# Kernel tuning notes

Hardware: AMD Instinct MI355X
Metric: run time of the kernel (lower is better)

The kernel has to match this reference:

```python
import jax, jax.numpy as jnp
import numpy as np

LN_EPS = 1e-5

def _conv2d(x, w, b, pad):
    # x: [B,C,H,W], w: [O,I,kh,kw] -> [B,O,H,W]
    y = jax.lax.conv_general_dilated(
        x, w, window_strides=(1, 1), padding=[(pad, pad), (pad, pad)],
        dimension_numbers=('NCHW', 'OIHW', 'NCHW'))
    return y + b[None, :, None, None]

def setup_inputs() -> dict:
    key = jax.random.key(0)
    ks = jax.random.split(key, 12)
    B, C, H, W = 4, 256, 64, 64
    D = 64  # inner_projection
    s_in = 1.0 / np.sqrt(C)
    s_d1 = 1.0 / np.sqrt(D)
    s_d3 = 1.0 / np.sqrt(D * 9)
    return {
        'x':     jax.random.normal(ks[0], (B, C, H, W), jnp.float32),
        'w_in':  jax.random.normal(ks[1], (D, C, 1, 1), jnp.float32) * s_in,
        'b_in':  jnp.zeros((D,), jnp.float32),
        'wq':    jax.random.normal(ks[2], (D, D, 3, 3), jnp.float32) * s_d3,
        'bq':    jnp.zeros((D,), jnp.float32),
        'wk':    jax.random.normal(ks[3], (D, D, 3, 3), jnp.float32) * s_d3,
        'bk':    jnp.zeros((D,), jnp.float32),
        'wv':    jax.random.normal(ks[4], (D, D, 3, 3), jnp.float32) * s_d3,
        'bv':    jnp.zeros((D,), jnp.float32),
        'w_out': jax.random.normal(ks[5], (C, D, 1, 1), jnp.float32) * s_d1,
        'b_out': jnp.zeros((C,), jnp.float32),
        'gamma': jax.random.normal(ks[6], (1,), jnp.float32) * 0.1,
        'ln_w':  jnp.ones((C,), jnp.float32),
        'ln_b':  jnp.zeros((C,), jnp.float32),
    }

def _attention(q, k, v):
    # full-pixel attention, NO 1/sqrt(d) scale (matches source)
    B, C, H, W = v.shape
    N = H * W
    qf = q.reshape(B, -1, N)   # [B,d,N]
    kf = k.reshape(B, -1, N)
    vf = v.reshape(B, -1, N)
    energy = jnp.einsum('bci,bcj->bij', qf, kf)      # [B,N,N] = Q^T K
    attn = jax.nn.softmax(energy, axis=-1)
    out = jnp.einsum('bcj,bij->bci', vf, attn)        # V @ attn^T
    return out.reshape(B, C, H, W)

def _layernorm2d(x, w, b):
    # normalize over channel dim per pixel (LayerNorm2d)
    mu = jnp.mean(x, axis=1, keepdims=True)
    var = jnp.var(x, axis=1, keepdims=True)
    xn = (x - mu) * jax.lax.rsqrt(var + LN_EPS)
    return xn * w[None, :, None, None] + b[None, :, None, None]

def reference(x, w_in, b_in, wq, bq, wk, bk, wv, bv, w_out, b_out, gamma, ln_w, ln_b):
    att = _conv2d(x, w_in, b_in, 0)          # inner projection [B,D,H,W]
    q = _conv2d(att, wq, bq, 1)
    k = _conv2d(att, wk, bk, 1)
    v = _conv2d(att, wv, bv, 1)
    att = _attention(q, k, v)
    att = _conv2d(att, w_out, b_out, 0)       # outer projection [B,C,H,W]
    return _layernorm2d(gamma * x + att, ln_w, ln_b)
```

## Files before the change

### kernel.cpp

```cpp
#include <hip/hip_runtime.h>
#include <hip/hip_bf16.h>

#define BB 4
#define CC 256
#define DD 64
#define HH 64
#define WW 64
#define NN 4096
#define NSPLIT 8
#define SM_SHIFT 64.0f

typedef __hip_bfloat16 bf16;
typedef __attribute__((ext_vector_type(8))) short bf16x8;
typedef __attribute__((ext_vector_type(4))) float f32x4;
typedef __attribute__((ext_vector_type(4))) short s16x4;

#define MFMA16(a, b, c) __builtin_amdgcn_mfma_f32_16x16x32_bf16(a, b, c, 0, 0, 0)

static __device__ __forceinline__ float ldin(const void* p, size_t i, bool isb) {
  return isb ? __bfloat162float(((const bf16*)p)[i]) : ((const float*)p)[i];
}
static __device__ __forceinline__ void stout(void* p, size_t i, float v, bool isb) {
  if (isb) ((bf16*)p)[i] = __float2bfloat16(v);
  else     ((float*)p)[i] = v;
}
static __device__ __forceinline__ unsigned pack2(bf16 a, bf16 b) {
  unsigned short ua = *reinterpret_cast<unsigned short*>(&a);
  unsigned short ub = *reinterpret_cast<unsigned short*>(&b);
  return (unsigned)ua | ((unsigned)ub << 16);
}
static __device__ __forceinline__ bool probe_bf16(const unsigned* lnw) {
  return lnw[0] == 0x3F803F80u;
}

__global__ __launch_bounds__(256) void k_wt(
    const void* __restrict__ wq, const void* __restrict__ wk,
    const void* __restrict__ wv, const void* __restrict__ w_in,
    const void* __restrict__ w_out,
    bf16* __restrict__ Wth, bf16* __restrict__ Wtl,
    bf16* __restrict__ Win_h, bf16* __restrict__ Win_l,
    bf16* __restrict__ Wo_h, bf16* __restrict__ Wo_l,
    const unsigned* __restrict__ lnw) {
  const bool isb = probe_bf16(lnw);
  int u = blockIdx.x * 256 + threadIdx.x;
  if (u < 110592) {
    int c3 = u / 36864, rem = u % 36864;
    int tap = rem / 4096, r2 = rem % 4096;
    int oc = r2 >> 6, ic = r2 & 63;
    const void* w = (c3 == 0) ? wq : ((c3 == 1) ? wk : wv);
    float v = ldin(w, (size_t)oc * 576 + ic * 9 + tap, isb);
    bf16 h = __float2bfloat16(v);
    Wth[u] = h;
    Wtl[u] = __float2bfloat16(v - __bfloat162float(h));
  } else if (u < 126976) {
    int v2 = u - 110592;
    float v = ldin(w_in, v2, isb);
    bf16 h = __float2bfloat16(v);
    Win_h[v2] = h;
    Win_l[v2] = __float2bfloat16(v - __bfloat162float(h));
  } else {
    int v2 = u - 126976;
    float v = ldin(w_out, v2, isb);
    bf16 h = __float2bfloat16(v);
    Wo_h[v2] = h;
    Wo_l[v2] = __float2bfloat16(v - __bfloat162float(h));
  }
}

__global__ __launch_bounds__(256) void k_conv_in(
    const void* __restrict__ x,
    const bf16* __restrict__ Win_h, const bf16* __restrict__ Win_l,
    const void* __restrict__ bias, bf16* __restrict__ att_h,
    bf16* __restrict__ att_l, const unsigned* __restrict__ lnw) {
  __shared__ __align__(16) short Xh[32 * 64];
  __shared__ __align__(16) short Xl[32 * 64];
  const bool isb = probe_bf16(lnw);
  const int b = blockIdx.y, n0 = blockIdx.x * 32;
  const int t = threadIdx.x;
  const int w = t >> 6, lane = t & 63, quad = lane >> 4, l16 = lane & 15;
  const int l7 = l16 & 7;
  const size_t xoff = (size_t)b * CC * NN;
  f32x4 acc[2];
  #pragma unroll
  for (int nt = 0; nt < 2; ++nt)
    #pragma unroll
    for (int r = 0; r < 4; ++r)
      acc[nt][r] = ldin(bias, w * 16 + quad * 4 + r, isb);
  for (int c0 = 0; c0 < CC; c0 += 64) {
    __syncthreads();
    #pragma unroll
    for (int i = 0; i < 4; ++i) {
      int u = t + i * 256;
      int dd = u >> 5, n = u & 31;
      float v0 = ldin(x, xoff + (size_t)(c0 + 2 * dd) * NN + n0 + n, isb);
      float v1 = ldin(x, xoff + (size_t)(c0 + 2 * dd + 1) * NN + n0 + n, isb);
      bf16 h0 = __float2bfloat16(v0), h1 = __float2bfloat16(v1);
      bf16 l0 = __float2bfloat16(v0 - __bfloat162float(h0));
      bf16 l1 = __float2bfloat16(v1 - __bfloat162float(h1));
      int cs = ((dd >> 2) ^ (n & 7)) * 8 + ((2 * dd) & 7);
      *(unsigned*)&Xh[n * 64 + cs] = pack2(h0, h1);
      *(unsigned*)&Xl[n * 64 + cs] = pack2(l0, l1);
    }
    __syncthreads();
    #pragma unroll
    for (int kc = 0; kc < 2; ++kc) {
      size_t woff = (size_t)(w * 16 + l16) * 256 + c0 + kc * 32 + quad * 8;
      bf16x8 wh = *(const bf16x8*)(Win_h + woff);
      bf16x8 wl = *(const bf16x8*)(Win_l + woff);
      const int xo = ((kc * 4 + quad) ^ l7) * 8;
      #pragma unroll
      for (int nt = 0; nt < 2; ++nt) {
        int rn = nt * 16 + l16;
        bf16x8 xh = *(const bf16x8*)&Xh[rn * 64 + xo];
        bf16x8 xl = *(const bf16x8*)&Xl[rn * 64 + xo];
        acc[nt] = MFMA16(wh, xh, acc[nt]);
        acc[nt] = MFMA16(wh, xl, acc[nt]);
        acc[nt] = MFMA16(wl, xh, acc[nt]);
      }
    }
  }
  #pragma unroll
  for (int nt = 0; nt < 2; ++nt) {
    size_t off = ((size_t)b * NN + n0 + nt * 16 + l16) * DD + w * 16 + quad * 4;
    bf16 h[4], l[4];
    #pragma unroll
    for (int r = 0; r < 4; ++r) {
      float v = acc[nt][r];
      h[r] = __float2bfloat16(v);
      l[r] = __float2bfloat16(v - __bfloat162float(h[r]));
    }
    *(uint2*)&att_h[off] = make_uint2(pack2(h[0], h[1]), pack2(h[2], h[3]));
    *(uint2*)&att_l[off] = make_uint2(pack2(l[0], l[1]), pack2(l[2], l[3]));
  }
}

__global__ __launch_bounds__(256) void k_conv3(
    const bf16* __restrict__ att_h, const bf16* __restrict__ att_l,
    const bf16* __restrict__ Wth, const bf16* __restrict__ Wtl,
    const void* __restrict__ bq, const void* __restrict__ bk,
    const void* __restrict__ bv,
    bf16* __restrict__ qth, bf16* __restrict__ qtl,
    bf16* __restrict__ kth, bf16* __restrict__ ktl,
    bf16* __restrict__ vt, const unsigned* __restrict__ lnw) {
  __shared__ __align__(16) short Ah[3 * 66 * 64];
  __shared__ __align__(16) short Al[3 * 66 * 64];
  float* o_s = reinterpret_cast<float*>(Ah);
  const bool isb = probe_bf16(lnw);
  const int y = blockIdx.x, b = blockIdx.y, c3 = blockIdx.z;
  const int t = threadIdx.x;
  const int w = t >> 6, lane = t & 63, quad = lane >> 4, l16 = lane & 15;
  const uint4 z4 = make_uint4(0, 0, 0, 0);
  #pragma unroll
  for (int r = 0; r < 3; ++r) {
    int yp = y + r - 1;
    bool ok = (unsigned)yp < 64u;
    const uint4* sh = (const uint4*)(att_h + ((size_t)b * NN + (size_t)yp * 64) * DD);
    const uint4* sl = (const uint4*)(att_l + ((size_t)b * NN + (size_t)yp * 64) * DD);
    #pragma unroll
    for (int ii = 0; ii < 2; ++ii) {
      int u = t + ii * 256;
      int xx = u >> 3, ch = u & 7;
      int rr = r * 66 + xx + 1;
      uint4 vh = ok ? sh[u] : z4;
      uint4 vl = ok ? sl[u] : z4;
      int cs = (ch ^ (rr & 7)) * 8;
      *(uint4*)&Ah[rr * 64 + cs] = vh;
      *(uint4*)&Al[rr * 64 + cs] = vl;
    }
    if (t < 16) {
      int rr = r * 66 + ((t & 1) ? 65 : 0);
      int cs = (t >> 1) * 8;
      *(uint4*)&Ah[rr * 64 + cs] = z4;
      *(uint4*)&Al[rr * 64 + cs] = z4;
    }
  }
  __syncthreads();
  const void* bp = (c3 == 0) ? bq : ((c3 == 1) ? bk : bv);
  const bf16* wth = Wth + (size_t)c3 * 9 * 4096;
  const bf16* wtl = Wtl + (size_t)c3 * 9 * 4096;
  f32x4 acc[4];
  #pragma unroll
  for (int nt = 0; nt < 4; ++nt)
    #pragma unroll
    for (int r = 0; r < 4; ++r)
      acc[nt][r] = ldin(bp, w * 16 + quad * 4 + r, isb);
  #pragma unroll
  for (int tap = 0; tap < 9; ++tap) {
    const int dy = tap / 3, dx = tap % 3;
    const int woff = tap * 4096 + (w * 16 + l16) * 64 + quad * 8;
    bf16x8 wh0 = *(const bf16x8*)(wth + woff);
    bf16x8 wh1 = *(const bf16x8*)(wth + woff + 32);
    bf16x8 wl0 = *(const bf16x8*)(wtl + woff);
    bf16x8 wl1 = *(const bf16x8*)(wtl + woff + 32);
    #pragma unroll
    for (int nt = 0; nt < 4; ++nt) {
      int rr = dy * 66 + nt * 16 + l16 + dx;
      int chA = (quad ^ (rr & 7)) * 8;
      int chB = ((quad + 4) ^ (rr & 7)) * 8;
      bf16x8 ah0 = *(const bf16x8*)&Ah[rr * 64 + chA];
      bf16x8 ah1 = *(const bf16x8*)&Ah[rr * 64 + chB];
      bf16x8 al0 = *(const bf16x8*)&Al[rr * 64 + chA];
      bf16x8 al1 = *(const bf16x8*)&Al[rr * 64 + chB];
      acc[nt] = MFMA16(wh0, ah0, acc[nt]);
      acc[nt] = MFMA16(wh1, ah1, acc[nt]);
      acc[nt] = MFMA16(wh0, al0, acc[nt]);
      acc[nt] = MFMA16(wh1, al1, acc[nt]);
      acc[nt] = MFMA16(wl0, ah0, acc[nt]);
      acc[nt] = MFMA16(wl1, ah1, acc[nt]);
    }
  }
  if (c3 < 2) {
    bf16* dh = (c3 == 0) ? qth : kth;
    bf16* dl = (c3 == 0) ? qtl : ktl;
    const size_t rowb = (size_t)b * NN + (size_t)y * 64;
    #pragma unroll
    for (int nt = 0; nt < 4; ++nt) {
      size_t off = (rowb + nt * 16 + l16) * DD + w * 16 + quad * 4;
      bf16 h[4], l[4];
      #pragma unroll
      for (int r = 0; r < 4; ++r) {
        float v = acc[nt][r];
        h[r] = __float2bfloat16(v);
        l[r] = __float2bfloat16(v - __bfloat162float(h[r]));
      }
      *(uint2*)&dh[off] = make_uint2(pack2(h[0], h[1]), pack2(h[2], h[3]));
      *(uint2*)&dl[off] = make_uint2(pack2(l[0], l[1]), pack2(l[2], l[3]));
    }
  } else {
    __syncthreads();
    #pragma unroll
    for (int nt = 0; nt < 4; ++nt)
      #pragma unroll
      for (int r = 0; r < 4; ++r)
        o_s[(nt * 16 + l16) * 65 + w * 16 + quad * 4 + r] = acc[nt][r];
    __syncthreads();
    #pragma unroll
    for (int i = 0; i < 8; ++i) {
      int u = t + i * 256;
      int c = u >> 5, np = (u & 31) * 2;
      float v0 = o_s[np * 65 + c], v1 = o_s[(np + 1) * 65 + c];
      *(unsigned*)&vt[((size_t)b * DD + c) * NN + (size_t)y * 64 + np] =
          pack2(__float2bfloat16(v0), __float2bfloat16(v1));
    }
  }
}

__global__ __launch_bounds__(256) void k_attn(
    const bf16* __restrict__ qth, const bf16* __restrict__ qtl,
    const bf16* __restrict__ kth, const bf16* __restrict__ ktl,
    const bf16* __restrict__ vt, float* __restrict__ po,
    float* __restrict__ pl) {
  __shared__ __align__(16) short Kh[64 * 64];
  __shared__ __align__(16) short Kl[64 * 64];
  __shared__ __align__(16) short Vs[64 * 64];
  __shared__ __align__(16) short Ps[64 * 64];
  const int b = blockIdx.y, i0 = blockIdx.x * 64, sp = blockIdx.z;
  const int jt0 = sp * (64 / NSPLIT), jt1 = jt0 + (64 / NSPLIT);
  const int t = threadIdx.x;
  const int w = t >> 6, lane = t & 63, quad = lane >> 4, l16 = lane & 15;
  const int l7 = l16 & 7;
  const int xA = (quad ^ l7) * 8;
  const int xB = ((quad + 4) ^ l7) * 8;
  const int sr = t >> 2, m4 = t & 3, sg = m4 * 16;
  const int sc0 = ((2 * m4) ^ (sr & 7)) * 8;
  const int sc1 = ((2 * m4 + 1) ^ (sr & 7)) * 8;
  {
    size_t off = ((size_t)b * NN + i0 + sr) * DD + sg;
    const uint4* qh = (const uint4*)(qth + off);
    const uint4* ql = (const uint4*)(qtl + off);
    *(uint4*)&Kh[sr * 64 + sc0] = qh[0];
    *(uint4*)&Kh[sr * 64 + sc1] = qh[1];
    *(uint4*)&Kl[sr * 64 + sc0] = ql[0];
    *(uint4*)&Kl[sr * 64 + sc1] = ql[1];
  }
  uint4 kh0, kh1, kl0, kl1, vx0, vx1;
  {
    size_t koff = ((size_t)b * NN + jt0 * 64 + sr) * DD + sg;
    kh0 = ((const uint4*)(kth + koff))[0]; kh1 = ((const uint4*)(kth + koff))[1];
    kl0 = ((const uint4*)(ktl + koff))[0]; kl1 = ((const uint4*)(ktl + koff))[1];
    size_t voff = ((size_t)b * DD + sr) * NN + jt0 * 64 + sg;
    vx0 = ((const uint4*)(vt + voff))[0];  vx1 = ((const uint4*)(vt + voff))[1];
  }
  __syncthreads();
  const int rq = w * 16 + l16;
  const bf16x8 qf_h0 = *(const bf16x8*)&Kh[rq * 64 + xA];
  const bf16x8 qf_h1 = *(const bf16x8*)&Kh[rq * 64 + xB];
  const bf16x8 qf_l0 = *(const bf16x8*)&Kl[rq * 64 + xA];
  const bf16x8 qf_l1 = *(const bf16x8*)&Kl[rq * 64 + xB];
  float l_run = 0.f;
  f32x4 oacc[4] = {};
  for (int jt = jt0; jt < jt1; ++jt) {
    __syncthreads();
    *(uint4*)&Kh[sr * 64 + sc0] = kh0;    *(uint4*)&Kh[sr * 64 + sc1] = kh1;
    *(uint4*)&Kl[sr * 64 + sc0] = kl0;    *(uint4*)&Kl[sr * 64 + sc1] = kl1;
    *(uint4*)&Vs[sr * 64 + sc0] = vx0;    *(uint4*)&Vs[sr * 64 + sc1] = vx1;
    __syncthreads();
    if (jt < jt1 - 1) {
      int j0n = (jt + 1) * 64;
      size_t koff = ((size_t)b * NN + j0n + sr) * DD + sg;
      kh0 = ((const uint4*)(kth + koff))[0]; kh1 = ((const uint4*)(kth + koff))[1];
      kl0 = ((const uint4*)(ktl + koff))[0]; kl1 = ((const uint4*)(ktl + koff))[1];
      size_t voff = ((size_t)b * DD + sr) * NN + j0n + sg;
      vx0 = ((const uint4*)(vt + voff))[0];  vx1 = ((const uint4*)(vt + voff))[1];
    }
    f32x4 s[4];
    #pragma unroll
    for (int mt = 0; mt < 4; ++mt) {
      int r0 = (mt * 16 + l16) * 64;
      bf16x8 kf_h0 = *(const bf16x8*)&Kh[r0 + xA];
      bf16x8 kf_h1 = *(const bf16x8*)&Kh[r0 + xB];
      bf16x8 kf_l0 = *(const bf16x8*)&Kl[r0 + xA];
      bf16x8 kf_l1 = *(const bf16x8*)&Kl[r0 + xB];
      f32x4 c = {0.f, 0.f, 0.f, 0.f};
      c = MFMA16(kf_h0, qf_h0, c);
      c = MFMA16(kf_h1, qf_h1, c);
      c = MFMA16(kf_h0, qf_l0, c);
      c = MFMA16(kf_h1, qf_l1, c);
      c = MFMA16(kf_l0, qf_h0, c);
      c = MFMA16(kf_l1, qf_h1, c);
      s[mt] = c;
    }
    float psum = 0.f;
    short pb[16];
    #pragma unroll
    for (int mt = 0; mt < 4; ++mt)
      #pragma unroll
      for (int r = 0; r < 4; ++r) {
        float p = __expf(s[mt][r] - SM_SHIFT);
        bf16 ph = __float2bfloat16(p);
        psum += __bfloat162float(ph);
        pb[mt * 4 + r] = *reinterpret_cast<short*>(&ph);
      }
    psum += __shfl_xor(psum, 16, 64);
    psum += __shfl_xor(psum, 32, 64);
    l_run += psum;
    #pragma unroll
    for (int mt = 0; mt < 4; ++mt) {
      s16x4 pk;
      pk.x = pb[mt * 4 + 0]; pk.y = pb[mt * 4 + 1];
      pk.z = pb[mt * 4 + 2]; pk.w = pb[mt * 4 + 3];
      int chP = ((2 * mt + (quad >> 1)) ^ l7) * 8 + (quad & 1) * 4;
      *(s16x4*)&Ps[rq * 64 + chP] = pk;
    }
    bf16x8 pf0 = *(const bf16x8*)&Ps[rq * 64 + xA];
    bf16x8 pf1 = *(const bf16x8*)&Ps[rq * 64 + xB];
    #pragma unroll
    for (int mt = 0; mt < 4; ++mt) {
      int r0 = (mt * 16 + l16) * 64;
      bf16x8 vf0 = *(const bf16x8*)&Vs[r0 + xA];
      bf16x8 vf1 = *(const bf16x8*)&Vs[r0 + xB];
      oacc[mt] = MFMA16(vf0, pf0, oacc[mt]);
      oacc[mt] = MFMA16(vf1, pf1, oacc[mt]);
    }
  }
  const int ig = i0 + w * 16 + l16;
  const size_t SEGC = (size_t)BB * DD * NN;
  #pragma unroll
  for (int mt = 0; mt < 4; ++mt)
    #pragma unroll
    for (int r = 0; r < 4; ++r) {
      int c = mt * 16 + quad * 4 + r;
      po[(size_t)sp * SEGC + ((size_t)b * DD + c) * NN + ig] = oacc[mt][r];
    }
  if (quad == 0) pl[((size_t)sp * BB + b) * NN + ig] = l_run;
}

__global__ __launch_bounds__(256) void k_out_ln(
    const float* __restrict__ po, const float* __restrict__ pl,
    const void* __restrict__ x,
    const bf16* __restrict__ Wo_h, const bf16* __restrict__ Wo_l,
    const void* __restrict__ bias, const void* __restrict__ gamma,
    const void* __restrict__ lw, const void* __restrict__ lb,
    void* __restrict__ out, const unsigned* __restrict__ lnw) {
  __shared__ __align__(16) short Ahs[32 * 64];
  __shared__ __align__(16) short Als[32 * 64];
  __shared__ float inv_s[32];
  __shared__ float red1[32 * 4], red2[32 * 4];
  __shared__ float mu_s[32], rs_s[32];
  __shared__ float lw_s[256], lb_s[256];
  const bool isb = probe_bf16(lnw);
  const int b = blockIdx.y, n0 = blockIdx.x * 32;
  const int t = threadIdx.x;
  const int w = t >> 6, lane = t & 63, quad = lane >> 4, l16 = lane & 15;
  const int l7 = l16 & 7;
  const size_t SEGC = (size_t)BB * DD * NN;
  if (t < 32) {
    int i = n0 + t;
    float lsum = 0.f;
    #pragma unroll
    for (int s = 0; s < NSPLIT; ++s) lsum += pl[((size_t)s * BB + b) * NN + i];
    inv_s[t] = 1.f / lsum;
  }
  lw_s[t] = ldin(lw, t, isb);
  lb_s[t] = ldin(lb, t, isb);
  const float g = ldin(gamma, 0, isb);
  __syncthreads();
  #pragma unroll
  for (int i = 0; i < 4; ++i) {
    int u = t + i * 256;
    int dd = u >> 5, n = u & 31;
    size_t base = ((size_t)b * DD + 2 * dd) * NN + n0 + n;
    float v0 = 0.f, v1 = 0.f;
    #pragma unroll
    for (int s = 0; s < NSPLIT; ++s) {
      v0 += po[(size_t)s * SEGC + base];
      v1 += po[(size_t)s * SEGC + base + NN];
    }
    float inv = inv_s[n];
    v0 *= inv; v1 *= inv;
    bf16 h0 = __float2bfloat16(v0), h1 = __float2bfloat16(v1);
    bf16 l0 = __float2bfloat16(v0 - __bfloat162float(h0));
    bf16 l1 = __float2bfloat16(v1 - __bfloat162float(h1));
    int cs = ((dd >> 2) ^ (n & 7)) * 8 + ((2 * dd) & 7);
    *(unsigned*)&Ahs[n * 64 + cs] = pack2(h0, h1);
    *(unsigned*)&Als[n * 64 + cs] = pack2(l0, l1);
  }
  f32x4 acc[4][2];
  #pragma unroll
  for (int oct = 0; oct < 4; ++oct)
    #pragma unroll
    for (int r = 0; r < 4; ++r) {
      float bo = ldin(bias, w * 64 + oct * 16 + quad * 4 + r, isb);
      #pragma unroll
      for (int nt = 0; nt < 2; ++nt) acc[oct][nt][r] = bo;
    }
  __syncthreads();
  #pragma unroll
  for (int oct = 0; oct < 4; ++oct) {
    const int base = w * 64 + oct * 16;
    #pragma unroll
    for (int kc = 0; kc < 2; ++kc) {
      size_t woff = (size_t)(base + l16) * 64 + kc * 32 + quad * 8;
      bf16x8 wh = *(const bf16x8*)(Wo_h + woff);
      bf16x8 wl = *(const bf16x8*)(Wo_l + woff);
      const int xo = ((kc * 4 + quad) ^ l7) * 8;
      #pragma unroll
      for (int nt = 0; nt < 2; ++nt) {
        int rn = nt * 16 + l16;
        bf16x8 ah = *(const bf16x8*)&Ahs[rn * 64 + xo];
        bf16x8 al = *(const bf16x8*)&Als[rn * 64 + xo];
        acc[oct][nt] = MFMA16(wh, ah, acc[oct][nt]);
        acc[oct][nt] = MFMA16(wh, al, acc[oct][nt]);
        acc[oct][nt] = MFMA16(wl, ah, acc[oct][nt]);
      }
    }
  }
  #pragma unroll
  for (int nt = 0; nt < 2; ++nt) {
    int nn = nt * 16 + l16;
    float s1 = 0.f, s2 = 0.f;
    #pragma unroll
    for (int oct = 0; oct < 4; ++oct)
      #pragma unroll
      for (int r = 0; r < 4; ++r) {
        int oc = w * 64 + oct * 16 + quad * 4 + r;
        float xv = ldin(x, ((size_t)b * CC + oc) * NN + n0 + nn, isb);
        float y = acc[oct][nt][r] + g * xv;
        acc[oct][nt][r] = y;
        s1 += y; s2 += y * y;
      }
    s1 += __shfl_xor(s1, 16, 64); s1 += __shfl_xor(s1, 32, 64);
    s2 += __shfl_xor(s2, 16, 64); s2 += __shfl_xor(s2, 32, 64);
    if (quad == 0) { red1[nn * 4 + w] = s1; red2[nn * 4 + w] = s2; }
  }
  __syncthreads();
  if (t < 32) {
    float sm = red1[t * 4] + red1[t * 4 + 1] + red1[t * 4 + 2] + red1[t * 4 + 3];
    float sq = red2[t * 4] + red2[t * 4 + 1] + red2[t * 4 + 2] + red2[t * 4 + 3];
    float mu = sm * (1.f / 256.f);
    float var = sq * (1.f / 256.f) - mu * mu;
    mu_s[t] = mu;
    rs_s[t] = rsqrtf(var + 1e-5f);
  }
  __syncthreads();
  #pragma unroll
  for (int nt = 0; nt < 2; ++nt) {
    int nn = nt * 16 + l16;
    float mu = mu_s[nn], rs = rs_s[nn];
    #pragma unroll
    for (int oct = 0; oct < 4; ++oct)
      #pragma unroll
      for (int r = 0; r < 4; ++r) {
        int oc = w * 64 + oct * 16 + quad * 4 + r;
        float o = (acc[oct][nt][r] - mu) * rs * lw_s[oc] + lb_s[oc];
        stout(out, ((size_t)b * CC + oc) * NN + n0 + nn, o, isb);
      }
  }
}

extern "C" void kernel_launch(void* const* d_in, const int* in_sizes, int n_in,
                              void* d_out, int out_size, void* d_ws, size_t ws_size,
                              hipStream_t stream) {
  const void* x     = d_in[0];
  const void* w_in  = d_in[1];
  const void* b_in  = d_in[2];
  const void* wq    = d_in[3];
  const void* bq    = d_in[4];
  const void* wk    = d_in[5];
  const void* bk    = d_in[6];
  const void* wv    = d_in[7];
  const void* bv    = d_in[8];
  const void* w_out = d_in[9];
  const void* b_out = d_in[10];
  const void* gamma = d_in[11];
  const void* ln_w  = d_in[12];
  const void* ln_b  = d_in[13];

  const size_t SEG = (size_t)BB * DD * NN;
  char*  p     = (char*)d_ws;
  bf16*  att_h = (bf16*)p;  p += SEG * 2;
  bf16*  att_l = (bf16*)p;  p += SEG * 2;
  bf16*  qth   = (bf16*)p;  p += SEG * 2;
  bf16*  qtl   = (bf16*)p;  p += SEG * 2;
  bf16*  kth   = (bf16*)p;  p += SEG * 2;
  bf16*  ktl   = (bf16*)p;  p += SEG * 2;
  bf16*  vt    = (bf16*)p;  p += SEG * 2;
  float* po    = (float*)p; p += (size_t)NSPLIT * SEG * 4;
  float* pl    = (float*)p; p += (size_t)NSPLIT * BB * NN * 4;
  bf16*  Wth   = (bf16*)p;  p += 110592 * 2;
  bf16*  Wtl   = (bf16*)p;  p += 110592 * 2;
  bf16*  Win_h = (bf16*)p;  p += 16384 * 2;
  bf16*  Win_l = (bf16*)p;  p += 16384 * 2;
  bf16*  Wo_h  = (bf16*)p;  p += 16384 * 2;
  bf16*  Wo_l  = (bf16*)p;  p += 16384 * 2;
  const unsigned* lnw = (const unsigned*)ln_w;

  k_wt<<<560, 256, 0, stream>>>(wq, wk, wv, w_in, w_out, Wth, Wtl,
                                Win_h, Win_l, Wo_h, Wo_l, lnw);
  k_conv_in<<<dim3(NN / 32, BB), 256, 0, stream>>>(x, Win_h, Win_l, b_in,
                                                   att_h, att_l, lnw);
  k_conv3<<<dim3(64, BB, 3), 256, 0, stream>>>(att_h, att_l, Wth, Wtl,
                                               bq, bk, bv,
                                               qth, qtl, kth, ktl, vt, lnw);
  k_attn<<<dim3(NN / 64, BB, NSPLIT), 256, 0, stream>>>(qth, qtl, kth, ktl, vt,
                                                        po, pl);
  k_out_ln<<<dim3(NN / 32, BB), 256, 0, stream>>>(po, pl, x, Wo_h, Wo_l,
                                                  b_out, gamma, ln_w, ln_b,
                                                  d_out, lnw);
}
```

Before: 186.1 us.

## Fuse weight prep into input conv, store attention partials as bf16, shrink out tile

Merges the weight-splitting kernel into the input 1x1 conv kernel and adds extra blocks for the conv3 and out weights. The conv now splits w_in into hi/lo on the fly, which removes one launch and the Win buffers. Attention split partial outputs are written in bf16 instead of fp32, halving that intermediate traffic at some precision cost. The output/LayerNorm kernel tile drops from 32 to 16 pixels, doubling its block count for occupancy.

```diff
diff --git a/kernel.cpp b/kernel.cpp
--- a/kernel.cpp
+++ b/kernel.cpp
@@ -32,51 +32,53 @@
 static __device__ __forceinline__ bool probe_bf16(const unsigned* lnw) {
   return lnw[0] == 0x3F803F80u;
 }
-
-__global__ __launch_bounds__(256) void k_wt(
+static __device__ __forceinline__ void split8(const float* v, bf16x8& h8,
+                                              bf16x8& l8) {
+  #pragma unroll
+  for (int r = 0; r < 8; ++r) {
+    bf16 h = __float2bfloat16(v[r]);
+    float lo = v[r] - __bfloat162float(h);
+    bf16 l = __float2bfloat16(lo);
+    h8[r] = *reinterpret_cast<short*>(&h);
+    l8[r] = *reinterpret_cast<short*>(&l);
+  }
+}
+
+__global__ __launch_bounds__(256) void k_conv_in_wt(
+    const void* __restrict__ x, const void* __restrict__ w_in,
+    const void* __restrict__ bias,
     const void* __restrict__ wq, const void* __restrict__ wk,
-    const void* __restrict__ wv, const void* __restrict__ w_in,
-    const void* __restrict__ w_out,
+    const void* __restrict__ wv, const void* __restrict__ w_out,
+    bf16* __restrict__ att_h, bf16* __restrict__ att_l,
     bf16* __restrict__ Wth, bf16* __restrict__ Wtl,
-    bf16* __restrict__ Win_h, bf16* __restrict__ Win_l,
     bf16* __restrict__ Wo_h, bf16* __restrict__ Wo_l,
     const unsigned* __restrict__ lnw) {
   const bool isb = probe_bf16(lnw);
-  int u = blockIdx.x * 256 + threadIdx.x;
-  if (u < 110592) {
-    int c3 = u / 36864, rem = u % 36864;
-    int tap = rem / 4096, r2 = rem % 4096;
-    int oc = r2 >> 6, ic = r2 & 63;
-    const void* w = (c3 == 0) ? wq : ((c3 == 1) ? wk : wv);
-    float v = ldin(w, (size_t)oc * 576 + ic * 9 + tap, isb);
-    bf16 h = __float2bfloat16(v);
-    Wth[u] = h;
-    Wtl[u] = __float2bfloat16(v - __bfloat162float(h));
-  } else if (u < 126976) {
-    int v2 = u - 110592;
-    float v = ldin(w_in, v2, isb);
-    bf16 h = __float2bfloat16(v);
-    Win_h[v2] = h;
-    Win_l[v2] = __float2bfloat16(v - __bfloat162float(h));
-  } else {
-    int v2 = u - 126976;
-    float v = ldin(w_out, v2, isb);
-    bf16 h = __float2bfloat16(v);
-    Wo_h[v2] = h;
-    Wo_l[v2] = __float2bfloat16(v - __bfloat162float(h));
-  }
-}
-
-__global__ __launch_bounds__(256) void k_conv_in(
-    const void* __restrict__ x,
-    const bf16* __restrict__ Win_h, const bf16* __restrict__ Win_l,
-    const void* __restrict__ bias, bf16* __restrict__ att_h,
-    bf16* __restrict__ att_l, const unsigned* __restrict__ lnw) {
+  const int id = blockIdx.x;
+  const int t = threadIdx.x;
+  if (id >= 512) {
+    int u = (id - 512) * 256 + t;
+    if (u < 110592) {
+      int c3 = u / 36864, rem = u % 36864;
+      int tap = rem / 4096, r2 = rem % 4096;
+      int oc = r2 >> 6, ic = r2 & 63;
+      const void* w = (c3 == 0) ? wq : ((c3 == 1) ? wk : wv);
+      float v = ldin(w, (size_t)oc * 576 + ic * 9 + tap, isb);
+      bf16 h = __float2bfloat16(v);
+      Wth[u] = h;
+      Wtl[u] = __float2bfloat16(v - __bfloat162float(h));
+    } else {
+      int v2 = u - 110592;
+      float v = ldin(w_out, v2, isb);
+      bf16 h = __float2bfloat16(v);
+      Wo_h[v2] = h;
+      Wo_l[v2] = __float2bfloat16(v - __bfloat162float(h));
+    }
+    return;
+  }
   __shared__ __align__(16) short Xh[32 * 64];
   __shared__ __align__(16) short Xl[32 * 64];
-  const bool isb = probe_bf16(lnw);
-  const int b = blockIdx.y, n0 = blockIdx.x * 32;
-  const int t = threadIdx.x;
+  const int b = id >> 7, n0 = (id & 127) * 32;
   const int w = t >> 6, lane = t & 63, quad = lane >> 4, l16 = lane & 15;
   const int l7 = l16 & 7;
   const size_t xoff = (size_t)b * CC * NN;
@@ -105,8 +107,16 @@
     #pragma unroll
     for (int kc = 0; kc < 2; ++kc) {
       size_t woff = (size_t)(w * 16 + l16) * 256 + c0 + kc * 32 + quad * 8;
-      bf16x8 wh = *(const bf16x8*)(Win_h + woff);
-      bf16x8 wl = *(const bf16x8*)(Win_l + woff);
+      bf16x8 wh, wl;
+      if (isb) {
+        wh = *(const bf16x8*)((const bf16*)w_in + woff);
+      } else {
+        const float* wp = (const float*)w_in + woff;
+        float4 a0 = *(const float4*)wp;
+        float4 a1 = *(const float4*)(wp + 4);
+        float vv[8] = {a0.x, a0.y, a0.z, a0.w, a1.x, a1.y, a1.z, a1.w};
+        split8(vv, wh, wl);
+      }
       const int xo = ((kc * 4 + quad) ^ l7) * 8;
       #pragma unroll
       for (int nt = 0; nt < 2; ++nt) {
@@ -115,7 +125,7 @@
         bf16x8 xl = *(const bf16x8*)&Xl[rn * 64 + xo];
         acc[nt] = MFMA16(wh, xh, acc[nt]);
         acc[nt] = MFMA16(wh, xl, acc[nt]);
-        acc[nt] = MFMA16(wl, xh, acc[nt]);
+        if (!isb) acc[nt] = MFMA16(wl, xh, acc[nt]);
       }
     }
   }
@@ -248,7 +258,7 @@
 __global__ __launch_bounds__(256) void k_attn(
     const bf16* __restrict__ qth, const bf16* __restrict__ qtl,
     const bf16* __restrict__ kth, const bf16* __restrict__ ktl,
-    const bf16* __restrict__ vt, float* __restrict__ po,
+    const bf16* __restrict__ vt, bf16* __restrict__ po,
     float* __restrict__ pl) {
   __shared__ __align__(16) short Kh[64 * 64];
   __shared__ __align__(16) short Kl[64 * 64];
@@ -360,31 +370,32 @@
     #pragma unroll
     for (int r = 0; r < 4; ++r) {
       int c = mt * 16 + quad * 4 + r;
-      po[(size_t)sp * SEGC + ((size_t)b * DD + c) * NN + ig] = oacc[mt][r];
+      po[(size_t)sp * SEGC + ((size_t)b * DD + c) * NN + ig] =
+          __float2bfloat16(oacc[mt][r]);
     }
   if (quad == 0) pl[((size_t)sp * BB + b) * NN + ig] = l_run;
 }
 
 __global__ __launch_bounds__(256) void k_out_ln(
-    const float* __restrict__ po, const float* __restrict__ pl,
+    const bf16* __restrict__ po, const float* __restrict__ pl,
     const void* __restrict__ x,
     const bf16* __restrict__ Wo_h, const bf16* __restrict__ Wo_l,
     const void* __restrict__ bias, const void* __restrict__ gamma,
     const void* __restrict__ lw, const void* __restrict__ lb,
     void* __restrict__ out, const unsigned* __restrict__ lnw) {
-  __shared__ __align__(16) short Ahs[32 * 64];
-  __shared__ __align__(16) short Als[32 * 64];
-  __shared__ float inv_s[32];
-  __shared__ float red1[32 * 4], red2[32 * 4];
-  __shared__ float mu_s[32], rs_s[32];
+  __shared__ __align__(16) short Ahs[16 * 64];
+  __shared__ __align__(16) short Als[16 * 64];
+  __shared__ float inv_s[16];
+  __shared__ float red1[16 * 4], red2[16 * 4];
+  __shared__ float mu_s[16], rs_s[16];
   __shared__ float lw_s[256], lb_s[256];
   const bool isb = probe_bf16(lnw);
-  const int b = blockIdx.y, n0 = blockIdx.x * 32;
+  const int b = blockIdx.y, n0 = blockIdx.x * 16;
   const int t = threadIdx.x;
   const int w = t >> 6, lane = t & 63, quad = lane >> 4, l16 = lane & 15;
   const int l7 = l16 & 7;
   const size_t SEGC = (size_t)BB * DD * NN;
-  if (t < 32) {
+  if (t < 16) {
     int i = n0 + t;
     float lsum = 0.f;
     #pragma unroll
@@ -396,15 +407,15 @@
   const float g = ldin(gamma, 0, isb);
   __syncthreads();
   #pragma unroll
-  for (int i = 0; i < 4; ++i) {
+  for (int i = 0; i < 2; ++i) {
     int u = t + i * 256;
-    int dd = u >> 5, n = u & 31;
+    int dd = u >> 4, n = u & 15;
     size_t base = ((size_t)b * DD + 2 * dd) * NN + n0 + n;
     float v0 = 0.f, v1 = 0.f;
     #pragma unroll
     for (int s = 0; s < NSPLIT; ++s) {
-      v0 += po[(size_t)s * SEGC + base];
-      v1 += po[(size_t)s * SEGC + base + NN];
+      v0 += __bfloat162float(po[(size_t)s * SEGC + base]);
+      v1 += __bfloat162float(po[(size_t)s * SEGC + base + NN]);
     }
     float inv = inv_s[n];
     v0 *= inv; v1 *= inv;
@@ -415,15 +426,12 @@
     *(unsigned*)&Ahs[n * 64 + cs] = pack2(h0, h1);
     *(unsigned*)&Als[n * 64 + cs] = pack2(l0, l1);
   }
-  f32x4 acc[4][2];
+  f32x4 acc[4];
   #pragma unroll
   for (int oct = 0; oct < 4; ++oct)
     #pragma unroll
-    for (int r = 0; r < 4; ++r) {
-      float bo = ldin(bias, w * 64 + oct * 16 + quad * 4 + r, isb);
-      #pragma unroll
-      for (int nt = 0; nt < 2; ++nt) acc[oct][nt][r] = bo;
-    }
+    for (int r = 0; r < 4; ++r)
+      acc[oct][r] = ldin(bias, w * 64 + oct * 16 + quad * 4 + r, isb);
   __syncthreads();
   #pragma unroll
   for (int oct = 0; oct < 4; ++oct) {
@@ -434,20 +442,15 @@
       bf16x8 wh = *(const bf16x8*)(Wo_h + woff);
       bf16x8 wl = *(const bf16x8*)(Wo_l + woff);
       const int xo = ((kc * 4 + quad) ^ l7) * 8;
-      #pragma unroll
-      for (int nt = 0; nt < 2; ++nt) {
-        int rn = nt * 16 + l16;
-        bf16x8 ah = *(const bf16x8*)&Ahs[rn * 64 + xo];
-        bf16x8 al = *(const bf16x8*)&Als[rn * 64 + xo];
-        acc[oct][nt] = MFMA16(wh, ah, acc[oct][nt]);
-        acc[oct][nt] = MFMA16(wh, al, acc[oct][nt]);
-        acc[oct][nt] = MFMA16(wl, ah, acc[oct][nt]);
-      }
-    }
-  }
-  #pragma unroll
-  for (int nt = 0; nt < 2; ++nt) {
-    int nn = nt * 16 + l16;
+      bf16x8 ah = *(const bf16x8*)&Ahs[l16 * 64 + xo];
+      bf16x8 al = *(const bf16x8*)&Als[l16 * 64 + xo];
+      acc[oct] = MFMA16(wh, ah, acc[oct]);
+      acc[oct] = MFMA16(wh, al, acc[oct]);
+      acc[oct] = MFMA16(wl, ah, acc[oct]);
+    }
+  }
+  {
+    int nn = l16;
     float s1 = 0.f, s2 = 0.f;
     #pragma unroll
     for (int oct = 0; oct < 4; ++oct)
@@ -455,8 +458,8 @@
       for (int r = 0; r < 4; ++r) {
         int oc = w * 64 + oct * 16 + quad * 4 + r;
         float xv = ldin(x, ((size_t)b * CC + oc) * NN + n0 + nn, isb);
-        float y = acc[oct][nt][r] + g * xv;
-        acc[oct][nt][r] = y;
+        float y = acc[oct][r] + g * xv;
+        acc[oct][r] = y;
         s1 += y; s2 += y * y;
       }
     s1 += __shfl_xor(s1, 16, 64); s1 += __shfl_xor(s1, 32, 64);
@@ -464,7 +467,7 @@
     if (quad == 0) { red1[nn * 4 + w] = s1; red2[nn * 4 + w] = s2; }
   }
   __syncthreads();
-  if (t < 32) {
+  if (t < 16) {
     float sm = red1[t * 4] + red1[t * 4 + 1] + red1[t * 4 + 2] + red1[t * 4 + 3];
     float sq = red2[t * 4] + red2[t * 4 + 1] + red2[t * 4 + 2] + red2[t * 4 + 3];
     float mu = sm * (1.f / 256.f);
@@ -473,16 +476,15 @@
     rs_s[t] = rsqrtf(var + 1e-5f);
   }
   __syncthreads();
-  #pragma unroll
-  for (int nt = 0; nt < 2; ++nt) {
-    int nn = nt * 16 + l16;
+  {
+    int nn = l16;
     float mu = mu_s[nn], rs = rs_s[nn];
     #pragma unroll
     for (int oct = 0; oct < 4; ++oct)
       #pragma unroll
       for (int r = 0; r < 4; ++r) {
         int oc = w * 64 + oct * 16 + quad * 4 + r;
-        float o = (acc[oct][nt][r] - mu) * rs * lw_s[oc] + lb_s[oc];
+        float o = (acc[oct][r] - mu) * rs * lw_s[oc] + lb_s[oc];
         stout(out, ((size_t)b * CC + oc) * NN + n0 + nn, o, isb);
       }
   }
@@ -515,26 +517,23 @@
   bf16*  kth   = (bf16*)p;  p += SEG * 2;
   bf16*  ktl   = (bf16*)p;  p += SEG * 2;
   bf16*  vt    = (bf16*)p;  p += SEG * 2;
-  float* po    = (float*)p; p += (size_t)NSPLIT * SEG * 4;
+  bf16*  po    = (bf16*)p;  p += (size_t)NSPLIT * SEG * 2;
   float* pl    = (float*)p; p += (size_t)NSPLIT * BB * NN * 4;
   bf16*  Wth   = (bf16*)p;  p += 110592 * 2;
   bf16*  Wtl   = (bf16*)p;  p += 110592 * 2;
-  bf16*  Win_h = (bf16*)p;  p += 16384 * 2;
-  bf16*  Win_l = (bf16*)p;  p += 16384 * 2;
   bf16*  Wo_h  = (bf16*)p;  p += 16384 * 2;
   bf16*  Wo_l  = (bf16*)p;  p += 16384 * 2;
   const unsigned* lnw = (const unsigned*)ln_w;
 
-  k_wt<<<560, 256, 0, stream>>>(wq, wk, wv, w_in, w_out, Wth, Wtl,
-                                Win_h, Win_l, Wo_h, Wo_l, lnw);
-  k_conv_in<<<dim3(NN / 32, BB), 256, 0, stream>>>(x, Win_h, Win_l, b_in,
-                                                   att_h, att_l, lnw);
+  k_conv_in_wt<<<1008, 256, 0, stream>>>(x, w_in, b_in, wq, wk, wv, w_out,
+                                         att_h, att_l, Wth, Wtl, Wo_h, Wo_l,
+                                         lnw);
   k_conv3<<<dim3(64, BB, 3), 256, 0, stream>>>(att_h, att_l, Wth, Wtl,
                                                bq, bk, bv,
                                                qth, qtl, kth, ktl, vt, lnw);
   k_attn<<<dim3(NN / 64, BB, NSPLIT), 256, 0, stream>>>(qth, qtl, kth, ktl, vt,
                                                         po, pl);
-  k_out_ln<<<dim3(NN / 32, BB), 256, 0, stream>>>(po, pl, x, Wo_h, Wo_l,
+  k_out_ln<<<dim3(NN / 16, BB), 256, 0, stream>>>(po, pl, x, Wo_h, Wo_l,
                                                   b_out, gamma, ln_w, ln_b,
                                                   d_out, lnw);
 }
```

New measurement: 190.4 us. 1.02x slower.
